# Kernel optimization log

Hardware: AMD Instinct MI355X
Metric: run time of the kernel (lower is better)

## Reference

```python
import jax, jax.numpy as jnp
import numpy as np
from math import sqrt

L, H, D, HD, F, V, P = 8, 16, 1024, 64, 4096, 32000, 2048
B, S = 2, 2048
EPS = 1e-5


def _ln(x, g, b):
    m = jnp.mean(x, axis=-1, keepdims=True)
    v = jnp.mean((x - m) ** 2, axis=-1, keepdims=True)
    return (x - m) * jax.lax.rsqrt(v + EPS) * g + b


def setup_inputs() -> dict:
    key = jax.random.key(0)
    ks = jax.random.split(key, 12)
    w = 0.02
    return {
        'input_ids': jax.random.randint(ks[0], (B, S), 0, V),
        'tok_emb': jax.random.normal(ks[1], (V, D), jnp.float32) * w,
        'pos_emb': jax.random.normal(ks[2], (P, D), jnp.float32) * w,
        'emb_g': jnp.ones((D,), jnp.float32),
        'emb_b': jnp.zeros((D,), jnp.float32),
        'ln1_g': jnp.ones((L, D), jnp.float32),
        'ln1_b': jnp.zeros((L, D), jnp.float32),
        'ln2_g': jnp.ones((L, D), jnp.float32),
        'ln2_b': jnp.zeros((L, D), jnp.float32),
        'Wq': jax.random.normal(ks[3], (L, H, D, HD), jnp.float32) * w,
        'bq': jnp.zeros((L, H, HD), jnp.float32),
        'Wk': jax.random.normal(ks[4], (L, H, D, HD), jnp.float32) * w,
        'bk': jnp.zeros((L, H, HD), jnp.float32),
        'Wv': jax.random.normal(ks[5], (L, H, D, HD), jnp.float32) * w,
        'bv': jnp.zeros((L, H, HD), jnp.float32),
        'Wo': jax.random.normal(ks[6], (L, D, D), jnp.float32) * w,
        'bo': jnp.zeros((L, D), jnp.float32),
        'W1': jax.random.normal(ks[7], (L, D, F), jnp.float32) * w,
        'b1': jnp.zeros((L, F), jnp.float32),
        'W2': jax.random.normal(ks[8], (L, F, D), jnp.float32) * w,
        'b2': jnp.zeros((L, D), jnp.float32),
    }


def _encoder(input_ids, tok_emb, pos_emb, emb_g, emb_b, ln1_g, ln1_b, ln2_g,
             ln2_b, Wq, bq, Wk, bk, Wv, bv, Wo, bo, W1, b1, W2, b2):
    seq = input_ids.shape[-1]
    x = tok_emb[input_ids] + pos_emb[:seq][None, :, :]  # [B,S,D]
    x = _ln(x, emb_g, emb_b)  # dropout = identity (eval)

    scale = 1.0 / sqrt(HD)

    def layer(x, p):
        (g1, b1_, g2, b2_, wq, bq_, wk, bk_, wv, bv_, wo, bo_, w1, bb1, w2, bb2) = p
        h = _ln(x, g1, b1_)
        q = jnp.einsum('bsd,hdk->bhsk', h, wq) + bq_[:, None, :]
        k = jnp.einsum('bsd,hdk->bhsk', h, wk) + bk_[:, None, :]
        v = jnp.einsum('bsd,hdk->bhsk', h, wv) + bv_[:, None, :]
        scores = jnp.einsum('bhsk,bhtk->bhst', q, k) * scale
        w = jax.nn.softmax(scores, axis=-1)
        av = jnp.einsum('bhst,bhtk->bhsk', w, v)  # [B,H,S,hd]
        av = jnp.transpose(av, (0, 2, 1, 3)).reshape(x.shape[0], x.shape[1], D)
        x = x + jnp.einsum('bsd,de->bse', av, wo) + bo_
        h2 = _ln(x, g2, b2_)
        f = jax.nn.gelu(jnp.einsum('bsd,df->bsf', h2, w1) + bb1, approximate=False)
        x = x + jnp.einsum('bsf,fd->bsd', f, w2) + bb2
        return x, None

    xs = (ln1_g, ln1_b, ln2_g, ln2_b, Wq, bq, Wk, bk, Wv, bv, Wo, bo, W1, b1, W2, b2)
    x, _ = jax.lax.scan(layer, x, xs)
    return x


def reference(input_ids, tok_emb, pos_emb, emb_g, emb_b, ln1_g, ln1_b, ln2_g,
              ln2_b, Wq, bq, Wk, bk, Wv, bv, Wo, bo, W1, b1, W2, b2):
    return _encoder(input_ids, tok_emb, pos_emb, emb_g, emb_b, ln1_g, ln1_b,
                    ln2_g, ln2_b, Wq, bq, Wk, bk, Wv, bv, Wo, bo, W1, b1, W2, b2)
```

## Files before the change

kernel.cpp:

```cpp
#include <hip/hip_runtime.h>
#include <hip/hip_bf16.h>

#define L_ 8
#define H_ 16
#define D_ 1024
#define HD_ 64
#define F_ 4096
#define B_ 2
#define S_ 2048
#define NTOK (B_*S_)

typedef unsigned short u16;
typedef __bf16 bf16x8 __attribute__((ext_vector_type(8)));
typedef float f32x4 __attribute__((ext_vector_type(4)));

__device__ __forceinline__ u16 f2b(float f){ union{float f; unsigned u;} c; c.f = f; unsigned u = c.u; return (u16)((u + 0x7fffu + ((u>>16)&1u)) >> 16); }
__device__ __forceinline__ u16 f2b_fast(float f){ union{float f; unsigned u;} c; c.f = f; return (u16)((c.u + 0x8000u) >> 16); }
__device__ __forceinline__ float b2f(u16 x){ union{unsigned u; float f;} c; c.u = ((unsigned)x)<<16; return c.f; }

__device__ __forceinline__ void gload16(const u16* g, u16* l){
  __builtin_amdgcn_global_load_lds(
      (const __attribute__((address_space(1))) void*)g,
      (__attribute__((address_space(3))) void*)l,
      16 , 0 , 0 );
}

__device__ __forceinline__ void lds_fence(){
  asm volatile("s_waitcnt lgkmcnt(0)" ::: "memory");
  __builtin_amdgcn_sched_barrier(0);
}

#define WAITV_BAR(n) do { \
  asm volatile("s_waitcnt vmcnt(%0)" :: "i"(n) : "memory"); \
  __builtin_amdgcn_sched_barrier(0); \
  __builtin_amdgcn_s_barrier(); \
} while(0)

__device__ __forceinline__ void blk_reduce2(float& a, float& b, float* sm){
  for (int off=32; off>0; off>>=1){ a += __shfl_down(a,off); b += __shfl_down(b,off); }
  int w = threadIdx.x>>6, ln = threadIdx.x&63;
  if (ln==0){ sm[w]=a; sm[4+w]=b; }
  __syncthreads();
  a = sm[0]+sm[1]+sm[2]+sm[3];
  b = sm[4]+sm[5]+sm[6]+sm[7];
}

__global__ __launch_bounds__(256) void embed_ln(const int* __restrict__ ids,
    const float* __restrict__ tok, const float* __restrict__ pos,
    const float* __restrict__ g, const float* __restrict__ bb,
    float* __restrict__ x)
{
  __shared__ float sm[8];
  int row = blockIdx.x;
  int s   = row % S_;
  int id  = ids[row];
  int d0  = threadIdx.x*4;
  float4 t4 = *(const float4*)(tok + (size_t)id*D_ + d0);
  float4 p4 = *(const float4*)(pos + (size_t)s *D_ + d0);
  float4 v; v.x=t4.x+p4.x; v.y=t4.y+p4.y; v.z=t4.z+p4.z; v.w=t4.w+p4.w;
  float sum = (v.x+v.y)+(v.z+v.w);
  float sq  = v.x*v.x+v.y*v.y+v.z*v.z+v.w*v.w;
  blk_reduce2(sum, sq, sm);
  float mean = sum * (1.0f/D_);
  float var  = sq  * (1.0f/D_) - mean*mean;
  float inv  = rsqrtf(var + 1e-5f);
  float4 g4 = *(const float4*)(g + d0);
  float4 b4 = *(const float4*)(bb + d0);
  float4 o; o.x=(v.x-mean)*inv*g4.x+b4.x; o.y=(v.y-mean)*inv*g4.y+b4.y;
            o.z=(v.z-mean)*inv*g4.z+b4.z; o.w=(v.w-mean)*inv*g4.w+b4.w;
  *(float4*)(x + (size_t)row*D_ + d0) = o;
}

__global__ __launch_bounds__(256) void ln_f32_bf16(const float* __restrict__ x,
    const float* __restrict__ g, const float* __restrict__ bb, u16* __restrict__ out)
{
  __shared__ float sm[8];
  int row = blockIdx.x;
  int d0  = threadIdx.x*4;
  float4 v = *(const float4*)(x + (size_t)row*D_ + d0);
  float sum = (v.x+v.y)+(v.z+v.w);
  float sq  = v.x*v.x+v.y*v.y+v.z*v.z+v.w*v.w;
  blk_reduce2(sum, sq, sm);
  float mean = sum * (1.0f/D_);
  float var  = sq  * (1.0f/D_) - mean*mean;
  float inv  = rsqrtf(var + 1e-5f);
  float4 g4 = *(const float4*)(g + d0);
  float4 b4 = *(const float4*)(bb + d0);
  uint2 w;
  w.x = (unsigned)f2b((v.x-mean)*inv*g4.x+b4.x) | ((unsigned)f2b((v.y-mean)*inv*g4.y+b4.y)<<16);
  w.y = (unsigned)f2b((v.z-mean)*inv*g4.z+b4.z) | ((unsigned)f2b((v.w-mean)*inv*g4.w+b4.w)<<16);
  *(uint2*)(out + (size_t)row*D_ + d0) = w;
}

__global__ __launch_bounds__(256) void transpose_w(const float* __restrict__ src,
    u16* __restrict__ dst, int R, int C)
{
  __shared__ u16 tile[64*64];
  int c0 = blockIdx.x*64, r0 = blockIdx.y*64;
  int t = threadIdx.x;
  #pragma unroll
  for (int i=0;i<2;i++){
    int idx = t + i*256;
    int row = idx>>3, c8 = idx&7;
    const float* p = src + (size_t)(r0+row)*C + c0 + c8*8;
    float4 a = *(const float4*)p;
    float4 b = *(const float4*)(p+4);
    u16 tmp[8];
    tmp[0]=f2b(a.x); tmp[1]=f2b(a.y); tmp[2]=f2b(a.z); tmp[3]=f2b(a.w);
    tmp[4]=f2b(b.x); tmp[5]=f2b(b.y); tmp[6]=f2b(b.z); tmp[7]=f2b(b.w);
    int sw = (row&7) ^ ((row>>3)&7);
    *(uint4*)(&tile[row*64 + ((c8 ^ sw)<<3)]) = *(uint4*)tmp;
  }
  __syncthreads();
  #pragma unroll
  for (int i=0;i<2;i++){
    int idx = t + i*256;
    int oc = idx>>3, tc = idx&7;
    u16 tmp[8];
    #pragma unroll
    for (int j=0;j<8;j++){
      int rr = tc*8 + j;
      int sw = (rr&7) ^ ((rr>>3)&7);
      tmp[j] = tile[rr*64 + ((((oc>>3) ^ sw)<<3) | (oc&7))];
    }
    *(uint4*)(dst + (size_t)(c0+oc)*R + r0 + tc*8) = *(uint4*)tmp;
  }
}

__global__ __launch_bounds__(256) void qkv_repack(const float* __restrict__ Wq,
    const float* __restrict__ Wk, const float* __restrict__ Wv,
    u16* __restrict__ dst, int layer)
{
  __shared__ u16 tile[64*64];
  int z = blockIdx.y; int which = z >> 4, h = z & 15;
  const float* W = (which==0) ? Wq : (which==1) ? Wk : Wv;
  const float* src = W + ((size_t)(layer*H_ + h))*D_*HD_;
  int r0 = blockIdx.x*64;
  int t = threadIdx.x;
  #pragma unroll
  for (int i=0;i<2;i++){
    int idx = t + i*256;
    int row = idx>>3, c8 = idx&7;
    const float* p = src + (size_t)(r0+row)*HD_ + c8*8;
    float4 a = *(const float4*)p;
    float4 b = *(const float4*)(p+4);
    u16 tmp[8];
    tmp[0]=f2b(a.x); tmp[1]=f2b(a.y); tmp[2]=f2b(a.z); tmp[3]=f2b(a.w);
    tmp[4]=f2b(b.x); tmp[5]=f2b(b.y); tmp[6]=f2b(b.z); tmp[7]=f2b(b.w);
    int sw = (row&7) ^ ((row>>3)&7);
    *(uint4*)(&tile[row*64 + ((c8 ^ sw)<<3)]) = *(uint4*)tmp;
  }
  __syncthreads();
  #pragma unroll
  for (int i=0;i<2;i++){
    int idx = t + i*256;
    int oc = idx>>3, tc = idx&7;
    u16 tmp[8];
    #pragma unroll
    for (int j=0;j<8;j++){
      int rr = tc*8 + j;
      int sw = (rr&7) ^ ((rr>>3)&7);
      tmp[j] = tile[rr*64 + ((((oc>>3) ^ sw)<<3) | (oc&7))];
    }
    *(uint4*)(dst + (size_t)(which*1024 + h*64 + oc)*D_ + r0 + tc*8) = *(uint4*)tmp;
  }
}

__device__ __forceinline__ void epi_store(float v0,float v1,float v2,float v3,
    float* xres, u16* obf, size_t idx, int epi)
{
  if (epi==1){
    float4 t = *(float4*)(xres + idx);
    t.x += v0; t.y += v1; t.z += v2; t.w += v3;
    *(float4*)(xres + idx) = t;
  } else {
    if (epi==2){
      #define GELU_T(v) { float t2=(v)*(v); float u=(v)*fmaf(t2,0.044715f,1.0f); \
                          float e=exp2f(u*-2.3022082f); (v)=(v)*__builtin_amdgcn_rcpf(1.0f+e); }
      GELU_T(v0); GELU_T(v1); GELU_T(v2); GELU_T(v3);
      #undef GELU_T
    }
    uint2 w;
    w.x = (unsigned)f2b_fast(v0) | ((unsigned)f2b_fast(v1) << 16);
    w.y = (unsigned)f2b_fast(v2) | ((unsigned)f2b_fast(v3) << 16);
    *(uint2*)(obf + idx) = w;
  }
}

__global__ __launch_bounds__(256) void gemm_64x128(
    const u16* __restrict__ A, const u16* __restrict__ Bt,
    const float* __restrict__ bias0, float* __restrict__ xres,
    int M, int N, int K)
{
  __shared__ u16 As[64*64];
  __shared__ u16 Bs[128*64];
  const int tid = threadIdx.x;
  const int nbx = gridDim.x;
  const int nwg = nbx * gridDim.y;
  int bid = blockIdx.x + nbx*blockIdx.y;
  int nid = (bid & 7)*(nwg >> 3) + (bid >> 3);
  const int bm = (nid % nbx) * 64;
  const int bn = (nid / nbx) * 128;
  const int wv = tid>>6, ln = tid&63;
  const int wr = wv>>1, wc = wv&1;
  const int l15 = ln&15, lhi = ln>>4;
  const int l8 = ln>>3;
  const int c8s = (ln&7) ^ l8;
  f32x4 acc[2][4];
  const f32x4 zero4 = {0.f,0.f,0.f,0.f};
  #pragma unroll
  for (int i=0;i<2;i++)
    #pragma unroll
    for (int j=0;j<4;j++) acc[i][j] = zero4;

  for (int k0 = 0; k0 < K; k0 += 64) {
    #pragma unroll
    for (int i=0;i<2;i++){
      int row = wv*16 + i*8 + l8;
      gload16(A + (size_t)(bm+row)*K + k0 + c8s*8, &As[(wv*16 + i*8)*64]);
    }
    #pragma unroll
    for (int i=0;i<4;i++){
      int row = wv*32 + i*8 + l8;
      gload16(Bt + (size_t)(bn+row)*K + k0 + c8s*8, &Bs[(wv*32 + i*8)*64]);
    }
    __syncthreads();
    #pragma unroll
    for (int ks=0; ks<2; ks++){
      bf16x8 af[2], bfr[4];
      #pragma unroll
      for (int i=0;i<2;i++){
        int ra = wr*32 + i*16 + l15;
        af[i]  = *(const bf16x8*)(&As[ra*64 + (((ks*4+lhi) ^ (ra&7))<<3)]);
      }
      #pragma unroll
      for (int j=0;j<4;j++){
        int rb = wc*64 + j*16 + l15;
        bfr[j] = *(const bf16x8*)(&Bs[rb*64 + (((ks*4+lhi) ^ (rb&7))<<3)]);
      }
      #pragma unroll
      for (int i=0;i<2;i++)
        #pragma unroll
        for (int j=0;j<4;j++)
          acc[i][j] = __builtin_amdgcn_mfma_f32_16x16x32_bf16(bfr[j], af[i], acc[i][j], 0,0,0);
    }
    __syncthreads();
  }

  #pragma unroll
  for (int j=0;j<4;j++){
    int col0 = bn + wc*64 + j*16 + lhi*4;
    float4 bv4 = *(const float4*)(bias0 + col0);
    #pragma unroll
    for (int i=0;i<2;i++){
      int row = bm + wr*32 + i*16 + l15;
      size_t idx = (size_t)row*N + col0;
      float4 t = *(float4*)(xres + idx);
      t.x += acc[i][j][0] + bv4.x;
      t.y += acc[i][j][1] + bv4.y;
      t.z += acc[i][j][2] + bv4.z;
      t.w += acc[i][j][3] + bv4.w;
      *(float4*)(xres + idx) = t;
    }
  }
}

__global__ __launch_bounds__(512,2) void gemm256(
    const u16* __restrict__ A, const u16* __restrict__ Bt,
    const float* __restrict__ bias0, const float* __restrict__ bias1, const float* __restrict__ bias2,
    float* __restrict__ xres, u16* __restrict__ obf, u16* __restrict__ vTout,
    int M, int N, int K, int epi)
{
  __shared__ u16 As[2][256*64];
  __shared__ u16 Bs[2][256*64];
  const int tid = threadIdx.x;
  const int nbx = gridDim.x;
  const int nwg = nbx * gridDim.y;
  int bid = blockIdx.x + nbx*blockIdx.y;
  int nid = (bid & 7)*(nwg >> 3) + (bid >> 3);
  const int bm = (nid % nbx) * 256;
  const int bn = (nid / nbx) * 256;
  const int wv = tid>>6, ln = tid&63;
  const int wm = wv>>2, wn = wv&3;
  const int l15 = ln&15, lhi = ln>>4;
  const int l8 = ln>>3;
  const int c8s = (ln&7) ^ l8;

  f32x4 acc[2][2][4][2];
  const f32x4 zero4 = {0.f,0.f,0.f,0.f};
  #pragma unroll
  for (int a=0;a<2;a++)
    #pragma unroll
    for (int b=0;b<2;b++)
      #pragma unroll
      for (int i=0;i<4;i++)
        #pragma unroll
        for (int j=0;j<2;j++) acc[a][b][i][j] = zero4;

  const u16* aB0 = A  + (size_t)(bm + wv*16 + l8)*K + c8s*8;
  const u16* bB0 = Bt + (size_t)(bn + wv*16 + l8)*K + c8s*8;

  #define ISSUE(c, kt) do {                                                  \
    const u16* aB = aB0 + (size_t)(kt)*64;                                   \
    const u16* bB = bB0 + (size_t)(kt)*64;                                   \
    gload16(aB,                 &As[c][(wv*16      )*64]);                   \
    gload16(aB + (size_t)8*K,   &As[c][(wv*16 +   8)*64]);                   \
    gload16(bB,                 &Bs[c][(wv*16      )*64]);                   \
    gload16(bB + (size_t)8*K,   &Bs[c][(wv*16 +   8)*64]);                   \
    gload16(bB + (size_t)128*K, &Bs[c][(128 + wv*16    )*64]);               \
    gload16(bB + (size_t)136*K, &Bs[c][(128 + wv*16 + 8)*64]);               \
    gload16(aB + (size_t)128*K, &As[c][(128 + wv*16    )*64]);               \
    gload16(aB + (size_t)136*K, &As[c][(128 + wv*16 + 8)*64]);               \
  } while(0)

  #define READ_B(c) do {                                                     \
    _Pragma("unroll")                                                        \
    for (int qc=0;qc<2;qc++)                                                 \
      _Pragma("unroll")                                                      \
      for (int j=0;j<2;j++){                                                 \
        int rb = qc*128 + wn*32 + j*16 + l15;                                \
        _Pragma("unroll")                                                    \
        for (int ks=0;ks<2;ks++)                                             \
          bfr[qc][j][ks] = *(const bf16x8*)(&Bs[c][rb*64 + (((ks*4+lhi) ^ (rb&7))<<3)]); \
      }                                                                      \
  } while(0)

  #define READ_A(c, qr) do {                                                 \
    _Pragma("unroll")                                                        \
    for (int i=0;i<4;i++){                                                   \
      int ra = (qr)*128 + wm*64 + i*16 + l15;                                \
      _Pragma("unroll")                                                      \
      for (int ks=0;ks<2;ks++)                                               \
        af[i][ks] = *(const bf16x8*)(&As[c][ra*64 + (((ks*4+lhi) ^ (ra&7))<<3)]); \
    }                                                                        \
  } while(0)

  #define MFMA_Q(qr) do {                                                    \
    __builtin_amdgcn_s_setprio(1);                                           \
    _Pragma("unroll")                                                        \
    for (int ks=0;ks<2;ks++)                                                 \
      _Pragma("unroll")                                                      \
      for (int i=0;i<4;i++)                                                  \
        _Pragma("unroll")                                                    \
        for (int qc=0;qc<2;qc++)                                             \
          _Pragma("unroll")                                                  \
          for (int j=0;j<2;j++)                                              \
            acc[qr][qc][i][j] = __builtin_amdgcn_mfma_f32_16x16x32_bf16(     \
                bfr[qc][j][ks], af[i][ks], acc[qr][qc][i][j], 0,0,0);        \
    __builtin_amdgcn_s_setprio(0);                                           \
  } while(0)

  const int nt = K >> 6;
  ISSUE(0, 0);
  WAITV_BAR(2);
  for (int t=0; t<nt-1; ++t){
    int c = t&1;
    ISSUE(c^1, t+1);
    bf16x8 bfr[2][2][2], af[4][2];
    READ_B(c);
    READ_A(c, 0);
    MFMA_Q(0);
    WAITV_BAR(8);
    READ_A(c, 1);
    MFMA_Q(1);
    WAITV_BAR(2);
  }
  {
    int c = (nt-1)&1;
    bf16x8 bfr[2][2][2], af[4][2];
    READ_B(c);
    READ_A(c, 0);
    MFMA_Q(0);
    WAITV_BAR(0);
    READ_A(c, 1);
    MFMA_Q(1);
  }
  #undef ISSUE
  #undef READ_B
  #undef READ_A
  #undef MFMA_Q

  #pragma unroll
  for (int qc=0; qc<2; qc++)
    #pragma unroll
    for (int j=0;j<2;j++){
      int colbase = bn + qc*128;
      int col0 = colbase + wn*32 + j*16 + lhi*4;
      float4 bv4;
      if (bias1){
        const float* bp = (col0 < 1024) ? (bias0 + col0)
                        : (col0 < 2048) ? (bias1 + col0 - 1024)
                                        : (bias2 + col0 - 2048);
        bv4 = *(const float4*)bp;
      } else {
        bv4 = *(const float4*)(bias0 + col0);
      }
      #pragma unroll
      for (int qr=0; qr<2; qr++)
        #pragma unroll
        for (int i=0;i<4;i++){
          int row = bm + qr*128 + wm*64 + i*16 + l15;
          float v0 = acc[qr][qc][i][j][0]+bv4.x;
          float v1 = acc[qr][qc][i][j][1]+bv4.y;
          float v2 = acc[qr][qc][i][j][2]+bv4.z;
          float v3 = acc[qr][qc][i][j][3]+bv4.w;
          if (vTout && colbase >= 2048){
            int vcol = col0 - 2048;
            int hh = vcol >> 6, hd0 = vcol & 63;
            int bb_ = row >> 11, tk = row & (S_-1);
            u16* vd = vTout + ((size_t)((bb_*16 + hh)*64 + hd0))*S_ + tk;
            vd[0]        = f2b_fast(v0);
            vd[S_]       = f2b_fast(v1);
            vd[2*S_]     = f2b_fast(v2);
            vd[3*(size_t)S_] = f2b_fast(v3);
          } else {
            epi_store(v0, v1, v2, v3, xres, obf, (size_t)row*N + col0, epi);
          }
        }
    }
}

__global__ __launch_bounds__(256) void attn_fwd(const u16* __restrict__ qkv,
    const u16* __restrict__ vT, u16* __restrict__ att)
{
  __shared__ u16 Ks[2][64*64];
  __shared__ u16 Vs[2][64*64];
  __shared__ u16 Ps[4][2][16*64];
  const int tid = threadIdx.x, wv = tid>>6, ln = tid&63, l15 = ln&15, lhi = ln>>4;
  const int l8 = ln>>3;
  const int cs = (ln&7) ^ l8;
  int bid = blockIdx.x + 16*(blockIdx.y + 16*blockIdx.z);
  int nid = (bid & 7)*64 + (bid >> 3);
  const int qt = nid & 15, h = (nid >> 4) & 15, b = nid >> 8;
  const u16* qg = qkv + (size_t)b*S_*3072 + h*64;
  const u16* kg = qg + 1024;
  const u16* vtg = vT + ((size_t)(b*16 + h)*64)*S_;

  bf16x8 qfA[2], qfB[2];
  {
    const u16* qrA = qg + (size_t)(qt*128 + wv*32 + l15)*3072;
    const u16* qrB = qrA + (size_t)16*3072;
    u16 ta[16], tb[16];
    *(uint4*)(ta)   = *(const uint4*)(qrA + lhi*8);
    *(uint4*)(ta+8) = *(const uint4*)(qrA + 32 + lhi*8);
    *(uint4*)(tb)   = *(const uint4*)(qrB + lhi*8);
    *(uint4*)(tb+8) = *(const uint4*)(qrB + 32 + lhi*8);
    #pragma unroll
    for (int i=0;i<16;i++){ ta[i] = f2b_fast(b2f(ta[i]) * 0.18033688f);
                            tb[i] = f2b_fast(b2f(tb[i]) * 0.18033688f); }
    qfA[0] = *(const bf16x8*)(ta); qfA[1] = *(const bf16x8*)(ta+8);
    qfB[0] = *(const bf16x8*)(tb); qfB[1] = *(const bf16x8*)(tb+8);
  }
  const f32x4 zero4 = {0.f,0.f,0.f,0.f};
  f32x4 oaccA[4], oaccB[4];
  #pragma unroll
  for (int j=0;j<4;j++){ oaccA[j] = zero4; oaccB[j] = zero4; }
  float lsumA = 0.f, lsumB = 0.f;

  const int qsw = (l15&7)<<3;
  u16* PsA = &Ps[wv][0][l15*64];
  u16* PsB = &Ps[wv][1][l15*64];

  #define STAGE_KV(bufi, kti) do {                                            \
    _Pragma("unroll")                                                         \
    for (int i_=0;i_<2;i_++){                                                 \
      int r0_ = wv*8 + i_*32;                                                 \
      int row_ = r0_ + l8;                                                    \
      gload16(kg  + (size_t)((kti)*64+row_)*3072 + cs*8, &Ks[bufi][r0_*64]);  \
      gload16(vtg + (size_t)row_*S_ + (kti)*64 + cs*8,   &Vs[bufi][r0_*64]);  \
    }                                                                         \
  } while(0)

  STAGE_KV(0, 0);
  __syncthreads();
  int buf = 0;

  for (int kt=0; kt<S_/64; kt++){
    if (kt+1 < S_/64) STAGE_KV(buf^1, kt+1);

    f32x4 sA[4], sB[4];
    __builtin_amdgcn_s_setprio(1);
    #pragma unroll
    for (int j=0;j<4;j++){
      sA[j] = zero4; sB[j] = zero4;
      #pragma unroll
      for (int ks=0; ks<2; ks++){
        int kr = j*16 + l15;
        bf16x8 kf = *(const bf16x8*)(&Ks[buf][kr*64 + (((ks*4+lhi) ^ (kr&7))<<3)]);
        sA[j] = __builtin_amdgcn_mfma_f32_16x16x32_bf16(kf, qfA[ks], sA[j], 0,0,0);
        sB[j] = __builtin_amdgcn_mfma_f32_16x16x32_bf16(kf, qfB[ks], sB[j], 0,0,0);
      }
    }
    __builtin_amdgcn_s_setprio(0);

    float partA = 0.f, partB = 0.f;
    #pragma unroll
    for (int j=0;j<4;j++){
      float a0 = exp2f(sA[j][0]), a1 = exp2f(sA[j][1]), a2 = exp2f(sA[j][2]), a3 = exp2f(sA[j][3]);
      float b0 = exp2f(sB[j][0]), b1 = exp2f(sB[j][1]), b2 = exp2f(sB[j][2]), b3 = exp2f(sB[j][3]);
      partA += (a0+a1)+(a2+a3);
      partB += (b0+b1)+(b2+b3);
      unsigned wA0, wA1, wB0, wB1;
      asm("v_cvt_pk_bf16_f32 %0, %1, %2" : "=v"(wA0) : "v"(a0), "v"(a1));
      asm("v_cvt_pk_bf16_f32 %0, %1, %2" : "=v"(wA1) : "v"(a2), "v"(a3));
      asm("v_cvt_pk_bf16_f32 %0, %1, %2" : "=v"(wB0) : "v"(b0), "v"(b1));
      asm("v_cvt_pk_bf16_f32 %0, %1, %2" : "=v"(wB1) : "v"(b2), "v"(b3));
      int e0 = (j*16 + lhi*4) ^ qsw;
      *(unsigned*)(PsA + e0)     = wA0;
      *(unsigned*)(PsA + e0 + 2) = wA1;
      *(unsigned*)(PsB + e0)     = wB0;
      *(unsigned*)(PsB + e0 + 2) = wB1;
    }
    lsumA += partA; lsumB += partB;

    lds_fence();

    bf16x8 pfA[2], pfB[2];
    pfA[0] = *(const bf16x8*)(PsA + ((lhi     ^ (l15&7))<<3));
    pfA[1] = *(const bf16x8*)(PsA + (((4+lhi) ^ (l15&7))<<3));
    pfB[0] = *(const bf16x8*)(PsB + ((lhi     ^ (l15&7))<<3));
    pfB[1] = *(const bf16x8*)(PsB + (((4+lhi) ^ (l15&7))<<3));

    __builtin_amdgcn_s_setprio(1);
    #pragma unroll
    for (int dj=0; dj<4; dj++){
      #pragma unroll
      for (int ks=0; ks<2; ks++){
        int vr = dj*16 + l15;
        bf16x8 vf = *(const bf16x8*)(&Vs[buf][vr*64 + (((ks*4+lhi) ^ (vr&7))<<3)]);
        oaccA[dj] = __builtin_amdgcn_mfma_f32_16x16x32_bf16(pfA[ks], vf, oaccA[dj], 0,0,0);
        oaccB[dj] = __builtin_amdgcn_mfma_f32_16x16x32_bf16(pfB[ks], vf, oaccB[dj], 0,0,0);
      }
    }
    __builtin_amdgcn_s_setprio(0);
    __syncthreads();
    buf ^= 1;
  }
  #undef STAGE_KV

  float totA = lsumA + __shfl_xor(lsumA, 16); totA += __shfl_xor(totA, 32);
  float totB = lsumB + __shfl_xor(lsumB, 16); totB += __shfl_xor(totB, 32);
  float invA[4], invB[4];
  #pragma unroll
  for (int r=0;r<4;r++){
    invA[r] = __builtin_amdgcn_rcpf(__shfl(totA, lhi*4+r));
    invB[r] = __builtin_amdgcn_rcpf(__shfl(totB, lhi*4+r));
  }

  #pragma unroll
  for (int dj=0; dj<4; dj++){
    #pragma unroll
    for (int r=0;r<4;r++){
      int q = lhi*4 + r;
      int tokA = qt*128 + wv*32 + q;
      int tokB = tokA + 16;
      att[(size_t)(b*S_ + tokA)*D_ + h*HD_ + dj*16 + l15] = f2b_fast(oaccA[dj][r] * invA[r]);
      att[(size_t)(b*S_ + tokB)*D_ + h*HD_ + dj*16 + l15] = f2b_fast(oaccB[dj][r] * invB[r]);
    }
  }
}

extern "C" void kernel_launch(void* const* d_in, const int* in_sizes, int n_in,
                              void* d_out, int out_size, void* d_ws, size_t ws_size,
                              hipStream_t stream)
{
  const int*   ids   = (const int*)d_in[0];
  const float* tok   = (const float*)d_in[1];
  const float* pos   = (const float*)d_in[2];
  const float* emb_g = (const float*)d_in[3];
  const float* emb_b = (const float*)d_in[4];
  const float* ln1g  = (const float*)d_in[5];
  const float* ln1b  = (const float*)d_in[6];
  const float* ln2g  = (const float*)d_in[7];
  const float* ln2b  = (const float*)d_in[8];
  const float* Wq = (const float*)d_in[9];
  const float* bq = (const float*)d_in[10];
  const float* Wk = (const float*)d_in[11];
  const float* bk = (const float*)d_in[12];
  const float* Wv = (const float*)d_in[13];
  const float* bv = (const float*)d_in[14];
  const float* Wo = (const float*)d_in[15];
  const float* bo = (const float*)d_in[16];
  const float* W1 = (const float*)d_in[17];
  const float* b1 = (const float*)d_in[18];
  const float* W2 = (const float*)d_in[19];
  const float* b2 = (const float*)d_in[20];

  float* x = (float*)d_out;
  char* ws = (char*)d_ws;
  u16* h     = (u16*)(ws);
  u16* qkvb  = (u16*)(ws + 8388608);
  u16* att   = (u16*)(ws + 33554432);
  u16* fbuf  = (u16*)(ws + 41943040);
  u16* vT    = fbuf;
  u16* wqkvt = (u16*)(ws + 75497472);
  u16* wot   = (u16*)(ws + 81788928);
  u16* w1t   = (u16*)(ws + 83886080);
  u16* w2t   = (u16*)(ws + 92274688);

  embed_ln<<<NTOK, 256, 0, stream>>>(ids, tok, pos, emb_g, emb_b, x);

  for (int l=0; l<L_; l++){
    ln_f32_bf16<<<NTOK, 256, 0, stream>>>(x, ln1g + l*D_, ln1b + l*D_, h);
    qkv_repack<<<dim3(16,48), 256, 0, stream>>>(Wq, Wk, Wv, wqkvt, l);
    gemm256<<<dim3(16,12), 512, 0, stream>>>(h, wqkvt,
        bq + l*1024, bk + l*1024, bv + l*1024,
        nullptr, qkvb, vT, NTOK, 3072, 1024, 0);
    attn_fwd<<<dim3(S_/128, H_, B_), 256, 0, stream>>>(qkvb, vT, att);
    transpose_w<<<dim3(16,16), 256, 0, stream>>>(Wo + (size_t)l*D_*D_, wot, D_, D_);
    gemm_64x128<<<dim3(64,8), 256, 0, stream>>>(att, wot,
        bo + l*D_, x, NTOK, 1024, 1024);
    ln_f32_bf16<<<NTOK, 256, 0, stream>>>(x, ln2g + l*D_, ln2b + l*D_, h);
    transpose_w<<<dim3(64,16), 256, 0, stream>>>(W1 + (size_t)l*D_*F_, w1t, D_, F_);
    gemm256<<<dim3(16,16), 512, 0, stream>>>(h, w1t,
        b1 + l*F_, nullptr, nullptr,
        nullptr, fbuf, nullptr, NTOK, 4096, 1024, 2);
    transpose_w<<<dim3(16,64), 256, 0, stream>>>(W2 + (size_t)l*F_*D_, w2t, F_, D_);
    gemm_64x128<<<dim3(64,8), 256, 0, stream>>>(fbuf, w2t,
        b2 + l*D_, x, NTOK, 1024, 4096);
  }
}
```

Measured before the change: 2.145 ms.

## Double-buffer LDS in residual GEMM to overlap global loads with MFMA

The 64x128 residual-add GEMM kernel now keeps two LDS buffers for A and B. It issues the async global-to-LDS loads for the next K tile before computing the current one, and splits each tile's compute into two phases separated by partial vmcnt waits and barriers. MFMA sections are wrapped in s_setprio to raise wave priority during math. The aim is to hide global memory latency behind compute. The cost is doubled LDS per block, which may lower occupancy, and more delicate wait and barrier accounting.

```diff
diff --git a/kernel.cpp b/kernel.cpp
--- a/kernel.cpp
+++ b/kernel.cpp
@@ -192,8 +192,8 @@
     const float* __restrict__ bias0, float* __restrict__ xres,
     int M, int N, int K)
 {
-  __shared__ u16 As[64*64];
-  __shared__ u16 Bs[128*64];
+  __shared__ u16 As[2][64*64];
+  __shared__ u16 Bs[2][128*64];
   const int tid = threadIdx.x;
   const int nbx = gridDim.x;
   const int nwg = nbx * gridDim.y;
@@ -213,39 +213,60 @@
     #pragma unroll
     for (int j=0;j<4;j++) acc[i][j] = zero4;
 
-  for (int k0 = 0; k0 < K; k0 += 64) {
-    #pragma unroll
-    for (int i=0;i<2;i++){
-      int row = wv*16 + i*8 + l8;
-      gload16(A + (size_t)(bm+row)*K + k0 + c8s*8, &As[(wv*16 + i*8)*64]);
-    }
-    #pragma unroll
-    for (int i=0;i<4;i++){
-      int row = wv*32 + i*8 + l8;
-      gload16(Bt + (size_t)(bn+row)*K + k0 + c8s*8, &Bs[(wv*32 + i*8)*64]);
-    }
-    __syncthreads();
-    #pragma unroll
-    for (int ks=0; ks<2; ks++){
-      bf16x8 af[2], bfr[4];
-      #pragma unroll
-      for (int i=0;i<2;i++){
-        int ra = wr*32 + i*16 + l15;
-        af[i]  = *(const bf16x8*)(&As[ra*64 + (((ks*4+lhi) ^ (ra&7))<<3)]);
-      }
-      #pragma unroll
-      for (int j=0;j<4;j++){
-        int rb = wc*64 + j*16 + l15;
-        bfr[j] = *(const bf16x8*)(&Bs[rb*64 + (((ks*4+lhi) ^ (rb&7))<<3)]);
-      }
-      #pragma unroll
-      for (int i=0;i<2;i++)
-        #pragma unroll
-        for (int j=0;j<4;j++)
-          acc[i][j] = __builtin_amdgcn_mfma_f32_16x16x32_bf16(bfr[j], af[i], acc[i][j], 0,0,0);
-    }
-    __syncthreads();
-  }
+  const u16* aB0 = A  + (size_t)(bm + wv*16 + l8)*K + c8s*8;
+  const u16* bB0 = Bt + (size_t)(bn + wv*32 + l8)*K + c8s*8;
+
+  #define ISSUE64(c, kt) do {                                                 \
+    const u16* aB = aB0 + (size_t)(kt)*64;                                    \
+    const u16* bB = bB0 + (size_t)(kt)*64;                                    \
+    gload16(bB,                &Bs[c][(wv*32      )*64]);                     \
+    gload16(bB + (size_t)8*K,  &Bs[c][(wv*32 +  8)*64]);                      \
+    gload16(bB + (size_t)16*K, &Bs[c][(wv*32 + 16)*64]);                      \
+    gload16(bB + (size_t)24*K, &Bs[c][(wv*32 + 24)*64]);                      \
+    gload16(aB,                &As[c][(wv*16      )*64]);                     \
+    gload16(aB + (size_t)8*K,  &As[c][(wv*16 +  8)*64]);                      \
+  } while(0)
+
+  #define PHASE64(c, ii) do {                                                 \
+    bf16x8 af_, bfr[4];                                                       \
+    {                                                                         \
+      int ra = wr*32 + (ii)*16 + l15;                                         \
+      _Pragma("unroll")                                                       \
+      for (int ks=0; ks<2; ks++){                                             \
+        af_ = *(const bf16x8*)(&As[c][ra*64 + (((ks*4+lhi) ^ (ra&7))<<3)]);   \
+        _Pragma("unroll")                                                     \
+        for (int j=0;j<4;j++){                                                \
+          int rb = wc*64 + j*16 + l15;                                        \
+          bfr[j] = *(const bf16x8*)(&Bs[c][rb*64 + (((ks*4+lhi) ^ (rb&7))<<3)]); \
+        }                                                                     \
+        __builtin_amdgcn_s_setprio(1);                                        \
+        _Pragma("unroll")                                                     \
+        for (int j=0;j<4;j++)                                                 \
+          acc[ii][j] = __builtin_amdgcn_mfma_f32_16x16x32_bf16(bfr[j], af_, acc[ii][j], 0,0,0); \
+        __builtin_amdgcn_s_setprio(0);                                        \
+      }                                                                       \
+    }                                                                         \
+  } while(0)
+
+  const int nt = K >> 6;
+  ISSUE64(0, 0);
+  WAITV_BAR(1);
+  for (int t=0; t<nt-1; ++t){
+    int c = t&1;
+    ISSUE64(c^1, t+1);
+    PHASE64(c, 0);
+    WAITV_BAR(6);
+    PHASE64(c, 1);
+    WAITV_BAR(1);
+  }
+  {
+    int c = (nt-1)&1;
+    PHASE64(c, 0);
+    WAITV_BAR(0);
+    PHASE64(c, 1);
+  }
+  #undef ISSUE64
+  #undef PHASE64
 
   #pragma unroll
   for (int j=0;j<4;j++){
```

After: 2.184 ms. Within noise of the previous version (+1.8%).
